# Kernel tuning notes

Hardware: AMD Instinct MI355X
Metric: run time of the kernel (lower is better)

## Reference

```python
import jax, jax.numpy as jnp
import numpy as np

N = 50000      # nodes
E = 400000     # edges (before self-loops)
G = 256        # graphs in batch
H = 2          # attention heads
C = 100        # out channels per head
F_IN = 336
SLOPE = 0.2    # PyG GATConv default negative_slope


def setup_inputs() -> dict:
    key = jax.random.key(0)
    ks = jax.random.split(key, 32)
    inp = {}
    inp['x'] = jax.random.normal(ks[0], (N, F_IN), dtype=jnp.float32)
    inp['edge_index'] = jax.random.randint(ks[1], (2, E), 0, N, dtype=jnp.int32)
    inp['batch'] = jnp.sort(jax.random.randint(ks[2], (N,), 0, G, dtype=jnp.int32))
    dims = [F_IN, 200, 200, 200, 200]
    k = 3
    for i in range(5):
        d = dims[i]
        inp[f'W{i+1}'] = jax.random.normal(ks[k], (d, H * C), dtype=jnp.float32) / float(np.sqrt(d)); k += 1
        inp[f'asrc{i+1}'] = jax.random.normal(ks[k], (H, C), dtype=jnp.float32) * 0.1; k += 1
        inp[f'adst{i+1}'] = jax.random.normal(ks[k], (H, C), dtype=jnp.float32) * 0.1; k += 1
        inp[f'bc{i+1}'] = jnp.zeros((H * C,), jnp.float32)
    for i, (a, b) in enumerate([(200, 100), (100, 100), (100, 29)]):
        inp[f'lw{i+1}'] = jax.random.normal(ks[k], (a, b), dtype=jnp.float32) / float(np.sqrt(a)); k += 1
        inp[f'lb{i+1}'] = jnp.zeros((b,), jnp.float32)
    return inp


def _gat(x, src, dst, W, a_s, a_d, b):
    # PyG GATConv (concat=True): per-head linear, additive attention,
    # softmax over incoming edges per destination node, weighted sum.
    h = (x @ W).reshape(-1, H, C)                      # [N,H,C]
    es = jnp.einsum('nhc,hc->nh', h, a_s)              # [N,H] src scores
    ed = jnp.einsum('nhc,hc->nh', h, a_d)              # [N,H] dst scores
    e = jax.nn.leaky_relu(es[src] + ed[dst], SLOPE)    # [E+N,H]
    m = jax.ops.segment_max(e, dst, num_segments=N)    # per-dest max (stable softmax)
    p = jnp.exp(e - m[dst])
    s = jax.ops.segment_sum(p, dst, num_segments=N)
    alpha = p / (s[dst] + 1e-16)                       # [E+N,H]
    msg = alpha[:, :, None] * h[src]                   # [E+N,H,C]
    out = jax.ops.segment_sum(msg, dst, num_segments=N)
    return out.reshape(-1, H * C) + b


def reference(x, edge_index, batch,
              W1, asrc1, adst1, bc1, W2, asrc2, adst2, bc2,
              W3, asrc3, adst3, bc3, W4, asrc4, adst4, bc4,
              W5, asrc5, adst5, bc5,
              lw1, lb1, lw2, lb2, lw3, lb3):
    loop = jnp.arange(N, dtype=edge_index.dtype)       # self-loops (PyG default)
    src = jnp.concatenate([edge_index[0], loop])
    dst = jnp.concatenate([edge_index[1], loop])
    for W, a_s, a_d, b in [(W1, asrc1, adst1, bc1), (W2, asrc2, adst2, bc2),
                           (W3, asrc3, adst3, bc3), (W4, asrc4, adst4, bc4),
                           (W5, asrc5, adst5, bc5)]:
        x = jax.nn.relu(_gat(x, src, dst, W, a_s, a_d, b))
    # global mean pool over nodes of each graph
    sums = jax.ops.segment_sum(x, batch, num_segments=G)
    cnt = jax.ops.segment_sum(jnp.ones((N, 1), x.dtype), batch, num_segments=G)
    x = sums / jnp.maximum(cnt, 1.0)
    x = jax.nn.relu(x @ lw1 + lb1)
    x = jax.nn.relu(x @ lw2 + lb2)
    return x @ lw3 + lb3
```

## Files before the change

### kernel.cpp

```cpp
#include <hip/hip_runtime.h>
#include <hip/hip_bf16.h>
#include <math.h>

#define F_IN   336
#define HC     200
#define Cch    100
#define SLOPE  0.2f
#define SCAN_BS 256

#define NPAD   224
#define KP0    352
#define KP1    224

using short8   = __attribute__((ext_vector_type(8))) short;
using float4v  = __attribute__((ext_vector_type(4))) float;
using ushort4v = __attribute__((ext_vector_type(4))) unsigned short;
using float2v  = __attribute__((ext_vector_type(2))) float;

__device__ inline unsigned short rne_bf16(float v) {
    unsigned int u = __float_as_uint(v);
    return (unsigned short)((u + 0x7fffu + ((u >> 16) & 1u)) >> 16);
}
__device__ inline void split_bf(float v, unsigned short& hi, unsigned short& lo) {
    hi = rne_bf16(v);
    float hv = __uint_as_float(((unsigned int)hi) << 16);
    lo = rne_bf16(v - hv);
}

__global__ void init_deg(int* deg, int n) {
    int i = blockIdx.x * 256 + threadIdx.x;
    if (i < n) deg[i] = 1;
}

__global__ void count_deg(const int* __restrict__ dst, int* deg, int e) {
    int i = blockIdx.x * 256 + threadIdx.x;
    if (i < e) atomicAdd(&deg[dst[i]], 1);
}

__global__ void scan_block(const int* __restrict__ deg, int* incl, int* bsums, int n) {
    __shared__ int sm[SCAN_BS];
    int i = blockIdx.x * SCAN_BS + threadIdx.x;
    int v = (i < n) ? deg[i] : 0;
    sm[threadIdx.x] = v;
    __syncthreads();
    for (int off = 1; off < SCAN_BS; off <<= 1) {
        int t = (threadIdx.x >= off) ? sm[threadIdx.x - off] : 0;
        __syncthreads();
        sm[threadIdx.x] += t;
        __syncthreads();
    }
    if (i < n) incl[i] = sm[threadIdx.x];
    if (threadIdx.x == SCAN_BS - 1) bsums[blockIdx.x] = sm[threadIdx.x];
}

__global__ void scan_sums(int* bsums, int nb) {
    __shared__ int sm[SCAN_BS];
    int v = (threadIdx.x < nb) ? bsums[threadIdx.x] : 0;
    sm[threadIdx.x] = v;
    __syncthreads();
    for (int off = 1; off < SCAN_BS; off <<= 1) {
        int t = (threadIdx.x >= off) ? sm[threadIdx.x - off] : 0;
        __syncthreads();
        sm[threadIdx.x] += t;
        __syncthreads();
    }
    if (threadIdx.x < nb) bsums[threadIdx.x] = sm[threadIdx.x] - v;
}

__global__ void scan_final(const int* __restrict__ incl, const int* __restrict__ deg,
                           const int* __restrict__ bsums, int* row_ptr, int* cursor, int n) {
    int i = blockIdx.x * SCAN_BS + threadIdx.x;
    if (i < n) {
        int inc = incl[i] + bsums[i / SCAN_BS];
        int ex  = inc - deg[i];
        row_ptr[i] = ex;
        cursor[i]  = ex;
        if (i == n - 1) row_ptr[n] = inc;
    }
}

__global__ void fill_csr(const int* __restrict__ src, const int* __restrict__ dst,
                         int* cursor, int* col_src, int e, int n) {
    int i = blockIdx.x * 256 + threadIdx.x;
    int te = e + n;
    if (i >= te) return;
    int s, d;
    if (i < e) { s = src[i]; d = dst[i]; }
    else       { s = i - e;  d = i - e; }
    int pos = atomicAdd(&cursor[d], 1);
    col_src[pos] = s;
}

__global__ void conv_x(const float* __restrict__ x, unsigned short* __restrict__ Ah,
                       unsigned short* __restrict__ Al, int n_nodes) {
    int i = blockIdx.x * 256 + threadIdx.x;
    int tot = n_nodes * KP0;
    if (i >= tot) return;
    int row = i / KP0, col = i - row * KP0;
    float v = (col < F_IN) ? x[(size_t)row * F_IN + col] : 0.f;
    unsigned short hi, lo;
    split_bf(v, hi, lo);
    Ah[i] = hi; Al[i] = lo;
}

__global__ void conv_w(const float* __restrict__ W, unsigned short* __restrict__ Bh,
                       unsigned short* __restrict__ Bl, int K, int Kp) {
    int i = blockIdx.x * 256 + threadIdx.x;
    int tot = NPAD * Kp;
    if (i >= tot) return;
    int n = i / Kp, k = i - n * Kp;
    float v = (n < HC && k < K) ? W[(size_t)k * HC + n] : 0.f;
    unsigned short hi, lo;
    split_bf(v, hi, lo);
    Bh[i] = hi; Bl[i] = lo;
}

#define LDK 40
__global__ __launch_bounds__(256, 2) void gemm_split(
    const unsigned short* __restrict__ Ah, const unsigned short* __restrict__ Al,
    const unsigned short* __restrict__ Bh, const unsigned short* __restrict__ Bl,
    float* __restrict__ h, int M, int Kp)
{
    __shared__ unsigned short As[2][64][LDK];
    __shared__ unsigned short Bs[2][NPAD][LDK];
    int tid  = threadIdx.x;
    int wave = tid >> 6, lane = tid & 63;
    int quad = lane >> 4, l16 = lane & 15;
    int wm = (wave >> 1) * 32;
    int wn = (wave & 1) * 112;
    int r0 = blockIdx.x * 64;

    float4v acc[2][7];
#pragma unroll
    for (int mt = 0; mt < 2; mt++)
#pragma unroll
        for (int nt = 0; nt < 7; nt++)
            acc[mt][nt] = (float4v){0.f, 0.f, 0.f, 0.f};

    for (int k0 = 0; k0 < Kp; k0 += 32) {
#pragma unroll
        for (int i = 0; i < 2; i++) {
            int c = tid + 256 * i;
            int s = c >> 8;
            int cc = c & 255;
            int row = cc >> 2, kc = (cc & 3) * 8;
            const unsigned short* g = s ? Al : Ah;
            uint4 v = make_uint4(0u, 0u, 0u, 0u);
            int gr = r0 + row;
            if (gr < M) v = *(const uint4*)(g + (size_t)gr * Kp + k0 + kc);
            *(uint4*)&As[s][row][kc] = v;
        }
#pragma unroll
        for (int i = 0; i < 7; i++) {
            int c = tid + 256 * i;
            int s = (c >= 896) ? 1 : 0;
            int cc = c - s * 896;
            int row = cc >> 2, kc = (cc & 3) * 8;
            const unsigned short* g = s ? Bl : Bh;
            *(uint4*)&Bs[s][row][kc] = *(const uint4*)(g + (size_t)row * Kp + k0 + kc);
        }
        __syncthreads();

        short8 a_h[2], a_l[2];
#pragma unroll
        for (int mt = 0; mt < 2; mt++) {
            a_h[mt] = *(const short8*)&As[0][wm + mt * 16 + l16][quad * 8];
            a_l[mt] = *(const short8*)&As[1][wm + mt * 16 + l16][quad * 8];
        }
#pragma unroll
        for (int nt = 0; nt < 7; nt++) {
            short8 b_h = *(const short8*)&Bs[0][wn + nt * 16 + l16][quad * 8];
            short8 b_l = *(const short8*)&Bs[1][wn + nt * 16 + l16][quad * 8];
#pragma unroll
            for (int mt = 0; mt < 2; mt++) {
                acc[mt][nt] = __builtin_amdgcn_mfma_f32_16x16x32_bf16(a_h[mt], b_h, acc[mt][nt], 0, 0, 0);
                acc[mt][nt] = __builtin_amdgcn_mfma_f32_16x16x32_bf16(a_h[mt], b_l, acc[mt][nt], 0, 0, 0);
                acc[mt][nt] = __builtin_amdgcn_mfma_f32_16x16x32_bf16(a_l[mt], b_h, acc[mt][nt], 0, 0, 0);
            }
        }
        __syncthreads();
    }

#pragma unroll
    for (int mt = 0; mt < 2; mt++) {
#pragma unroll
        for (int nt = 0; nt < 7; nt++) {
            int col = wn + nt * 16 + l16;
            if (col >= HC) continue;
#pragma unroll
            for (int r = 0; r < 4; r++) {
                int grow = r0 + wm + mt * 16 + quad * 4 + r;
                if (grow < M) h[(size_t)grow * HC + col] = acc[mt][nt][r];
            }
        }
    }
}

__global__ __launch_bounds__(256) void gat_scores(
    const float* __restrict__ h, const float* __restrict__ asrc, const float* __restrict__ adst,
    float* __restrict__ es, float* __restrict__ ed, int n_nodes)
{
    int wave = threadIdx.x >> 6, lane = threadIdx.x & 63;
    int n = blockIdx.x * 4 + wave;
    if (n >= n_nodes) return;
#pragma unroll
    for (int hd = 0; hd < 2; hd++) {
        const float* hr = h + (size_t)n * HC + hd * Cch;
        const float* as = asrc + hd * Cch;
        const float* ad = adst + hd * Cch;
        float v = hr[lane];
        float ps = v * as[lane];
        float pd = v * ad[lane];
        if (lane < Cch - 64) {
            float v2 = hr[lane + 64];
            ps += v2 * as[lane + 64];
            pd += v2 * ad[lane + 64];
        }
        for (int off = 32; off > 0; off >>= 1) {
            ps += __shfl_down(ps, off);
            pd += __shfl_down(pd, off);
        }
        if (lane == 0) { es[n * 2 + hd] = ps; ed[n * 2 + hd] = pd; }
    }
}

__global__ __launch_bounds__(256) void gat_alpha(
    const float* __restrict__ es, const float* __restrict__ ed,
    const int* __restrict__ row_ptr, const int* __restrict__ col_src,
    float* __restrict__ pbuf, float* __restrict__ linv, int n_nodes)
{
    int n = blockIdx.x * 256 + threadIdx.x;
    if (n >= n_nodes) return;
    int e0 = row_ptr[n], e1 = row_ptr[n + 1];
    float ed0 = ed[n * 2], ed1 = ed[n * 2 + 1];
    float m0 = -INFINITY, m1 = -INFINITY;
    for (int e = e0; e < e1; e++) {
        int s = col_src[e];
        float s0 = es[s * 2] + ed0, s1 = es[s * 2 + 1] + ed1;
        s0 = s0 > 0.f ? s0 : SLOPE * s0;
        s1 = s1 > 0.f ? s1 : SLOPE * s1;
        m0 = fmaxf(m0, s0); m1 = fmaxf(m1, s1);
    }
    float l0 = 0.f, l1 = 0.f;
    for (int e = e0; e < e1; e++) {
        int s = col_src[e];
        float s0 = es[s * 2] + ed0, s1 = es[s * 2 + 1] + ed1;
        s0 = s0 > 0.f ? s0 : SLOPE * s0;
        s1 = s1 > 0.f ? s1 : SLOPE * s1;
        float p0 = __expf(s0 - m0), p1 = __expf(s1 - m1);
        l0 += p0; l1 += p1;
        float2v pp = {p0, p1};
        *(float2v*)&pbuf[(size_t)e * 2] = pp;
    }
    linv[n * 2]     = 1.f / (l0 + 1e-16f);
    linv[n * 2 + 1] = 1.f / (l1 + 1e-16f);
}

template<bool WF, bool WB>
__global__ __launch_bounds__(256) void gat_gather(
    const float* __restrict__ h, const float* __restrict__ pbuf, const float* __restrict__ linv,
    const int* __restrict__ row_ptr, const int* __restrict__ col_src,
    const float* __restrict__ bias, float* __restrict__ outF,
    unsigned short* __restrict__ oh, unsigned short* __restrict__ ol, int n_nodes)
{
    int wave = threadIdx.x >> 6, lane = threadIdx.x & 63;
    int n = blockIdx.x * 4 + wave;
    if (n >= n_nodes) return;
    int e0 = row_ptr[n], e1 = row_ptr[n + 1];
    bool act  = lane < 50;
    int  hsel = (lane >= 25) ? 1 : 0;

    float4v a0 = {0.f, 0.f, 0.f, 0.f}, a1 = {0.f, 0.f, 0.f, 0.f};
    float4v a2 = {0.f, 0.f, 0.f, 0.f}, a3 = {0.f, 0.f, 0.f, 0.f};

    for (int cbase = e0; cbase < e1; cbase += 64) {
        int cnt = e1 - cbase; if (cnt > 64) cnt = 64;
        int   sidx = 0;
        float px = 0.f, py = 0.f;
        if (lane < cnt) {
            sidx = col_src[cbase + lane];
            float2v pp = *(const float2v*)&pbuf[(size_t)(cbase + lane) * 2];
            px = pp.x; py = pp.y;
        }
        int j = 0;
        for (; j + 4 <= cnt; j += 4) {
            int s0 = __shfl(sidx, j + 0), s1 = __shfl(sidx, j + 1);
            int s2 = __shfl(sidx, j + 2), s3 = __shfl(sidx, j + 3);
            float x0 = __shfl(px, j + 0), y0 = __shfl(py, j + 0);
            float x1 = __shfl(px, j + 1), y1 = __shfl(py, j + 1);
            float x2 = __shfl(px, j + 2), y2 = __shfl(py, j + 2);
            float x3 = __shfl(px, j + 3), y3 = __shfl(py, j + 3);
            float p0 = hsel ? y0 : x0;
            float p1 = hsel ? y1 : x1;
            float p2 = hsel ? y2 : x2;
            float p3 = hsel ? y3 : x3;
            if (act) {
                float4v v0 = *(const float4v*)(h + (size_t)s0 * HC + lane * 4);
                float4v v1 = *(const float4v*)(h + (size_t)s1 * HC + lane * 4);
                float4v v2 = *(const float4v*)(h + (size_t)s2 * HC + lane * 4);
                float4v v3 = *(const float4v*)(h + (size_t)s3 * HC + lane * 4);
                a0.x += p0 * v0.x; a0.y += p0 * v0.y; a0.z += p0 * v0.z; a0.w += p0 * v0.w;
                a1.x += p1 * v1.x; a1.y += p1 * v1.y; a1.z += p1 * v1.z; a1.w += p1 * v1.w;
                a2.x += p2 * v2.x; a2.y += p2 * v2.y; a2.z += p2 * v2.z; a2.w += p2 * v2.w;
                a3.x += p3 * v3.x; a3.y += p3 * v3.y; a3.z += p3 * v3.z; a3.w += p3 * v3.w;
            }
        }
        for (; j < cnt; j++) {
            int s0 = __shfl(sidx, j);
            float x0 = __shfl(px, j), y0 = __shfl(py, j);
            float p0 = hsel ? y0 : x0;
            if (act) {
                float4v v0 = *(const float4v*)(h + (size_t)s0 * HC + lane * 4);
                a0.x += p0 * v0.x; a0.y += p0 * v0.y; a0.z += p0 * v0.z; a0.w += p0 * v0.w;
            }
        }
    }
    float4v acc;
    acc.x = (a0.x + a1.x) + (a2.x + a3.x);
    acc.y = (a0.y + a1.y) + (a2.y + a3.y);
    acc.z = (a0.z + a1.z) + (a2.z + a3.z);
    acc.w = (a0.w + a1.w) + (a2.w + a3.w);

    float li = linv[n * 2 + hsel];
    if (act) {
        float4v bb = *(const float4v*)(bias + lane * 4);
        float4v r;
        r.x = fmaxf(acc.x * li + bb.x, 0.f);
        r.y = fmaxf(acc.y * li + bb.y, 0.f);
        r.z = fmaxf(acc.z * li + bb.z, 0.f);
        r.w = fmaxf(acc.w * li + bb.w, 0.f);
        if (WF) {
            __builtin_nontemporal_store(r, (float4v*)(outF + (size_t)n * HC + lane * 4));
        }
        if (WB) {
            ushort4v hv, lv;
            split_bf(r.x, ((unsigned short*)&hv)[0], ((unsigned short*)&lv)[0]);
            split_bf(r.y, ((unsigned short*)&hv)[1], ((unsigned short*)&lv)[1]);
            split_bf(r.z, ((unsigned short*)&hv)[2], ((unsigned short*)&lv)[2]);
            split_bf(r.w, ((unsigned short*)&hv)[3], ((unsigned short*)&lv)[3]);
            size_t b = (size_t)n * NPAD + lane * 4;
            __builtin_nontemporal_store(hv, (ushort4v*)(oh + b));
            __builtin_nontemporal_store(lv, (ushort4v*)(ol + b));
        }
    } else if (WB && lane < 56) {
        ushort4v z = {0, 0, 0, 0};
        size_t b = (size_t)n * NPAD + lane * 4;
        __builtin_nontemporal_store(z, (ushort4v*)(oh + b));
        __builtin_nontemporal_store(z, (ushort4v*)(ol + b));
    }
}

__global__ void pool_zero(float* pool, int tot) {
    int i = blockIdx.x * 256 + threadIdx.x;
    if (i < tot) pool[i] = 0.f;
}

__global__ __launch_bounds__(256) void pool_part(
    const float* __restrict__ x, const int* __restrict__ batch,
    float* __restrict__ pool, int n_nodes)
{
    int wave = threadIdx.x >> 6, lane = threadIdx.x & 63;
    int base = (blockIdx.x * 4 + wave) * 16;
    if (base >= n_nodes) return;
    bool act = lane < 50;
    int end = base + 16; if (end > n_nodes) end = n_nodes;
    float4v acc = {0.f, 0.f, 0.f, 0.f};
    int curg = batch[base];
    for (int n = base; n < end; n++) {
        int g = batch[n];
        if (g != curg) {
            if (act) {
                float* pp = pool + (size_t)curg * HC + lane * 4;
                atomicAdd(pp + 0, acc.x); atomicAdd(pp + 1, acc.y);
                atomicAdd(pp + 2, acc.z); atomicAdd(pp + 3, acc.w);
            }
            acc = (float4v){0.f, 0.f, 0.f, 0.f};
            curg = g;
        }
        if (act) {
            float4v v = *(const float4v*)(x + (size_t)n * HC + lane * 4);
            acc.x += v.x; acc.y += v.y; acc.z += v.z; acc.w += v.w;
        }
    }
    if (act) {
        float* pp = pool + (size_t)curg * HC + lane * 4;
        atomicAdd(pp + 0, acc.x); atomicAdd(pp + 1, acc.y);
        atomicAdd(pp + 2, acc.z); atomicAdd(pp + 3, acc.w);
    }
}

__global__ void pool_div(float* pool, const int* __restrict__ gstart, int g_count) {
    int i = blockIdx.x * 256 + threadIdx.x;
    if (i >= g_count * HC) return;
    int g = i / HC;
    float cnt = (float)(gstart[g + 1] - gstart[g]);
    pool[i] /= fmaxf(cnt, 1.f);
}

__global__ void graph_bounds(const int* __restrict__ batch, int* gstart, int n, int g) {
    int i = blockIdx.x * 256 + threadIdx.x;
    if (i >= n) return;
    int b = batch[i];
    int bp = (i == 0) ? -1 : batch[i - 1];
    for (int q = bp + 1; q <= b; q++) gstart[q] = i;
    if (i == n - 1) for (int q = b + 1; q <= g; q++) gstart[q] = n;
}

template<int KIN, int KOUT, bool RELU>
__global__ __launch_bounds__(128) void mlp(
    const float* __restrict__ in, const float* __restrict__ W, const float* __restrict__ b,
    float* __restrict__ out)
{
    __shared__ float xi[KIN];
    int g = blockIdx.x;
    for (int k = threadIdx.x; k < KIN; k += blockDim.x) xi[k] = in[g * KIN + k];
    __syncthreads();
    int j = threadIdx.x;
    if (j < KOUT) {
        float s = b[j];
        for (int k = 0; k < KIN; k++) s = fmaf(xi[k], W[k * KOUT + j], s);
        if (RELU) s = fmaxf(s, 0.f);
        out[g * KOUT + j] = s;
    }
}

extern "C" void kernel_launch(void* const* d_in, const int* in_sizes, int n_in,
                              void* d_out, int out_size, void* d_ws, size_t ws_size,
                              hipStream_t stream) {
    const float* x     = (const float*)d_in[0];
    const int*   ei    = (const int*)d_in[1];
    const int*   batch = (const int*)d_in[2];
    const float *W[5], *asrc[5], *adst[5], *bc[5];
    for (int i = 0; i < 5; i++) {
        W[i]    = (const float*)d_in[3 + i * 4];
        asrc[i] = (const float*)d_in[4 + i * 4];
        adst[i] = (const float*)d_in[5 + i * 4];
        bc[i]   = (const float*)d_in[6 + i * 4];
    }
    const float* lw1 = (const float*)d_in[23];
    const float* lb1 = (const float*)d_in[24];
    const float* lw2 = (const float*)d_in[25];
    const float* lb2 = (const float*)d_in[26];
    const float* lw3 = (const float*)d_in[27];
    const float* lb3 = (const float*)d_in[28];
    float* out = (float*)d_out;

    const int N  = in_sizes[0] / F_IN;
    const int E  = in_sizes[1] / 2;
    const int G  = out_size / 29;
    const int TE = E + N;
    const int* esrc = ei;
    const int* edst = ei + E;

    char* p = (char*)d_ws;
    auto carve = [&](size_t bytes) { void* r = (void*)p; p += ((bytes + 255) / 256) * 256; return r; };
    float*          hbuf = (float*)carve((size_t)N * HC * 4);
    unsigned short* Ah   = (unsigned short*)carve((size_t)N * KP0 * 2);
    unsigned short* Al   = (unsigned short*)carve((size_t)N * KP0 * 2);
    float*          outF = (float*)Ah;
    unsigned short* Wth  = (unsigned short*)carve((size_t)NPAD * KP0 * 2);
    unsigned short* Wtl  = (unsigned short*)carve((size_t)NPAD * KP0 * 2);
    float* es_     = (float*)carve((size_t)N * 2 * 4);
    float* ed_     = (float*)carve((size_t)N * 2 * 4);
    float* pbuf    = (float*)carve((size_t)TE * 2 * 4);
    float* linv    = (float*)carve((size_t)N * 2 * 4);
    int*   deg     = (int*)carve((size_t)N * 4);
    int*   incl    = (int*)carve((size_t)N * 4);
    int*   bsums   = (int*)carve(SCAN_BS * 4);
    int*   row_ptr = (int*)carve((size_t)(N + 1) * 4);
    int*   cursor  = (int*)carve((size_t)N * 4);
    int*   col_src = (int*)carve((size_t)TE * 4);
    int*   gstart  = (int*)carve((size_t)(G + 1) * 4);
    float* pool    = (float*)carve((size_t)G * HC * 4);
    float* t1      = (float*)carve((size_t)G * 100 * 4);
    float* t2      = (float*)carve((size_t)G * 100 * 4);

    const int nBlkN   = (N + 255) / 256;
    const int nBlkE   = (E + 255) / 256;
    const int nBlkTE  = (TE + 255) / 256;
    const int nScanB  = (N + SCAN_BS - 1) / SCAN_BS;
    const int nWaveB  = (N + 3) / 4;
    const int nGemmB  = (N + 63) / 64;
    const int nPoolB  = (N + 63) / 64;

    init_deg<<<nBlkN, 256, 0, stream>>>(deg, N);
    count_deg<<<nBlkE, 256, 0, stream>>>(edst, deg, E);
    scan_block<<<nScanB, SCAN_BS, 0, stream>>>(deg, incl, bsums, N);
    scan_sums<<<1, SCAN_BS, 0, stream>>>(bsums, nScanB);
    scan_final<<<nScanB, SCAN_BS, 0, stream>>>(incl, deg, bsums, row_ptr, cursor, N);
    fill_csr<<<nBlkTE, 256, 0, stream>>>(esrc, edst, cursor, col_src, E, N);

    conv_x<<<(N * KP0 + 255) / 256, 256, 0, stream>>>(x, Ah, Al, N);

    for (int L = 0; L < 5; L++) {
        int K  = (L == 0) ? F_IN : HC;
        int Kp = (L == 0) ? KP0 : KP1;
        conv_w<<<(NPAD * Kp + 255) / 256, 256, 0, stream>>>(W[L], Wth, Wtl, K, Kp);
        gemm_split<<<nGemmB, 256, 0, stream>>>(Ah, Al, Wth, Wtl, hbuf, N, Kp);
        gat_scores<<<nWaveB, 256, 0, stream>>>(hbuf, asrc[L], adst[L], es_, ed_, N);
        gat_alpha<<<nBlkN, 256, 0, stream>>>(es_, ed_, row_ptr, col_src, pbuf, linv, N);
        if (L < 4)
            gat_gather<false, true><<<nWaveB, 256, 0, stream>>>(hbuf, pbuf, linv, row_ptr, col_src,
                                                                bc[L], nullptr, Ah, Al, N);
        else
            gat_gather<true, false><<<nWaveB, 256, 0, stream>>>(hbuf, pbuf, linv, row_ptr, col_src,
                                                                bc[L], outF, nullptr, nullptr, N);
    }

    graph_bounds<<<nBlkN, 256, 0, stream>>>(batch, gstart, N, G);
    pool_zero<<<(G * HC + 255) / 256, 256, 0, stream>>>(pool, G * HC);
    pool_part<<<nPoolB, 256, 0, stream>>>(outF, batch, pool, N);
    pool_div<<<(G * HC + 255) / 256, 256, 0, stream>>>(pool, gstart, G);

    mlp<200, 100, true ><<<G, 128, 0, stream>>>(pool, lw1, lb1, t1);
    mlp<100, 100, true ><<<G, 128, 0, stream>>>(t1, lw2, lb2, t2);
    mlp<100, 29,  false><<<G, 128, 0, stream>>>(t2, lw3, lb3, out);
}
```

Before: 951.7 us.

## Fuse attention score dot products into GEMM epilogue and parallelize softmax per node

The GEMM epilogue now computes the per-node source and destination attention scores, reducing across lanes with shuffles and across waves with LDS atomics, which removes the separate gat_scores kernel and its re-read of h. The per-node softmax kernel now assigns 16 lanes per node instead of one thread, stores the leaky-relu scores in the first pass and reads them back to avoid gathering es twice. conv_x is vectorized to float4 loads and ushort4 stores. The changes add epilogue register pressure and atomic traffic in the GEMM, and the float4 load relies on the 336-column rows being 16-byte aligned.

```diff
diff --git a/kernel.cpp b/kernel.cpp
--- a/kernel.cpp
+++ b/kernel.cpp
@@ -93,14 +93,22 @@
 
 __global__ void conv_x(const float* __restrict__ x, unsigned short* __restrict__ Ah,
                        unsigned short* __restrict__ Al, int n_nodes) {
-    int i = blockIdx.x * 256 + threadIdx.x;
-    int tot = n_nodes * KP0;
+    const int GPR = KP0 / 4;
+    int i = blockIdx.x * 256 + threadIdx.x;
+    int tot = n_nodes * GPR;
     if (i >= tot) return;
-    int row = i / KP0, col = i - row * KP0;
-    float v = (col < F_IN) ? x[(size_t)row * F_IN + col] : 0.f;
-    unsigned short hi, lo;
-    split_bf(v, hi, lo);
-    Ah[i] = hi; Al[i] = lo;
+    int row = i / GPR, g4 = i - row * GPR;
+    int col = g4 * 4;
+    float4v v = {0.f, 0.f, 0.f, 0.f};
+    if (col < F_IN) v = *(const float4v*)(x + (size_t)row * F_IN + col);
+    ushort4v hv, lv;
+    split_bf(v.x, ((unsigned short*)&hv)[0], ((unsigned short*)&lv)[0]);
+    split_bf(v.y, ((unsigned short*)&hv)[1], ((unsigned short*)&lv)[1]);
+    split_bf(v.z, ((unsigned short*)&hv)[2], ((unsigned short*)&lv)[2]);
+    split_bf(v.w, ((unsigned short*)&hv)[3], ((unsigned short*)&lv)[3]);
+    size_t b = (size_t)row * KP0 + col;
+    *(ushort4v*)(Ah + b) = hv;
+    *(ushort4v*)(Al + b) = lv;
 }
 
 __global__ void conv_w(const float* __restrict__ W, unsigned short* __restrict__ Bh,
@@ -119,16 +127,21 @@
 __global__ __launch_bounds__(256, 2) void gemm_split(
     const unsigned short* __restrict__ Ah, const unsigned short* __restrict__ Al,
     const unsigned short* __restrict__ Bh, const unsigned short* __restrict__ Bl,
-    float* __restrict__ h, int M, int Kp)
+    const float* __restrict__ asrc, const float* __restrict__ adst,
+    float* __restrict__ h, float* __restrict__ es, float* __restrict__ ed,
+    int M, int Kp)
 {
     __shared__ unsigned short As[2][64][LDK];
     __shared__ unsigned short Bs[2][NPAD][LDK];
+    __shared__ float sc[64][4];
     int tid  = threadIdx.x;
     int wave = tid >> 6, lane = tid & 63;
     int quad = lane >> 4, l16 = lane & 15;
     int wm = (wave >> 1) * 32;
     int wn = (wave & 1) * 112;
     int r0 = blockIdx.x * 64;
+
+    ((float*)sc)[tid] = 0.f;
 
     float4v acc[2][7];
 #pragma unroll
@@ -181,79 +194,113 @@
         __syncthreads();
     }
 
+    float asc[7], adc[7];
+    bool  vld[7];
+    bool  hd1[7];
+#pragma unroll
+    for (int nt = 0; nt < 7; nt++) {
+        int col = wn + nt * 16 + l16;
+        vld[nt] = col < HC;
+        hd1[nt] = col >= Cch;
+        asc[nt] = vld[nt] ? asrc[col] : 0.f;
+        adc[nt] = vld[nt] ? adst[col] : 0.f;
+    }
+
 #pragma unroll
     for (int mt = 0; mt < 2; mt++) {
+        float p[4][4];
+#pragma unroll
+        for (int r = 0; r < 4; r++)
+#pragma unroll
+            for (int t = 0; t < 4; t++) p[r][t] = 0.f;
 #pragma unroll
         for (int nt = 0; nt < 7; nt++) {
             int col = wn + nt * 16 + l16;
-            if (col >= HC) continue;
 #pragma unroll
             for (int r = 0; r < 4; r++) {
+                float v = acc[mt][nt][r];
                 int grow = r0 + wm + mt * 16 + quad * 4 + r;
-                if (grow < M) h[(size_t)grow * HC + col] = acc[mt][nt][r];
+                if (vld[nt] && grow < M) h[(size_t)grow * HC + col] = v;
+                float va = v * asc[nt], vd = v * adc[nt];
+                p[r][0] += hd1[nt] ? 0.f : va;
+                p[r][1] += hd1[nt] ? va  : 0.f;
+                p[r][2] += hd1[nt] ? 0.f : vd;
+                p[r][3] += hd1[nt] ? vd  : 0.f;
             }
         }
-    }
-}
-
-__global__ __launch_bounds__(256) void gat_scores(
-    const float* __restrict__ h, const float* __restrict__ asrc, const float* __restrict__ adst,
-    float* __restrict__ es, float* __restrict__ ed, int n_nodes)
-{
-    int wave = threadIdx.x >> 6, lane = threadIdx.x & 63;
-    int n = blockIdx.x * 4 + wave;
-    if (n >= n_nodes) return;
-#pragma unroll
-    for (int hd = 0; hd < 2; hd++) {
-        const float* hr = h + (size_t)n * HC + hd * Cch;
-        const float* as = asrc + hd * Cch;
-        const float* ad = adst + hd * Cch;
-        float v = hr[lane];
-        float ps = v * as[lane];
-        float pd = v * ad[lane];
-        if (lane < Cch - 64) {
-            float v2 = hr[lane + 64];
-            ps += v2 * as[lane + 64];
-            pd += v2 * ad[lane + 64];
-        }
-        for (int off = 32; off > 0; off >>= 1) {
-            ps += __shfl_down(ps, off);
-            pd += __shfl_down(pd, off);
-        }
-        if (lane == 0) { es[n * 2 + hd] = ps; ed[n * 2 + hd] = pd; }
-    }
-}
-
-__global__ __launch_bounds__(256) void gat_alpha(
+#pragma unroll
+        for (int off = 1; off < 16; off <<= 1)
+#pragma unroll
+            for (int r = 0; r < 4; r++)
+#pragma unroll
+                for (int t = 0; t < 4; t++)
+                    p[r][t] += __shfl_xor(p[r][t], off);
+        if (l16 == 0) {
+            int lrow = wm + mt * 16 + quad * 4;
+#pragma unroll
+            for (int r = 0; r < 4; r++)
+#pragma unroll
+                for (int t = 0; t < 4; t++)
+                    atomicAdd(&sc[lrow + r][t], p[r][t]);
+        }
+    }
+    __syncthreads();
+    if (tid < 64) {
+        int grow = r0 + tid;
+        if (grow < M) {
+            es[grow * 2 + 0] = sc[tid][0];
+            es[grow * 2 + 1] = sc[tid][1];
+            ed[grow * 2 + 0] = sc[tid][2];
+            ed[grow * 2 + 1] = sc[tid][3];
+        }
+    }
+}
+
+__global__ __launch_bounds__(256) void gat_alpha_par(
     const float* __restrict__ es, const float* __restrict__ ed,
     const int* __restrict__ row_ptr, const int* __restrict__ col_src,
     float* __restrict__ pbuf, float* __restrict__ linv, int n_nodes)
 {
-    int n = blockIdx.x * 256 + threadIdx.x;
+    int tid = threadIdx.x;
+    int sub = tid >> 4;
+    int l   = tid & 15;
+    int n = blockIdx.x * 16 + sub;
     if (n >= n_nodes) return;
     int e0 = row_ptr[n], e1 = row_ptr[n + 1];
     float ed0 = ed[n * 2], ed1 = ed[n * 2 + 1];
     float m0 = -INFINITY, m1 = -INFINITY;
-    for (int e = e0; e < e1; e++) {
+    for (int e = e0 + l; e < e1; e += 16) {
         int s = col_src[e];
-        float s0 = es[s * 2] + ed0, s1 = es[s * 2 + 1] + ed1;
+        float2v q = *(const float2v*)&es[s * 2];
+        float s0 = q.x + ed0, s1 = q.y + ed1;
         s0 = s0 > 0.f ? s0 : SLOPE * s0;
         s1 = s1 > 0.f ? s1 : SLOPE * s1;
         m0 = fmaxf(m0, s0); m1 = fmaxf(m1, s1);
+        float2v w = {s0, s1};
+        *(float2v*)&pbuf[(size_t)e * 2] = w;
+    }
+#pragma unroll
+    for (int off = 1; off < 16; off <<= 1) {
+        m0 = fmaxf(m0, __shfl_xor(m0, off));
+        m1 = fmaxf(m1, __shfl_xor(m1, off));
     }
     float l0 = 0.f, l1 = 0.f;
-    for (int e = e0; e < e1; e++) {
-        int s = col_src[e];
-        float s0 = es[s * 2] + ed0, s1 = es[s * 2 + 1] + ed1;
-        s0 = s0 > 0.f ? s0 : SLOPE * s0;
-        s1 = s1 > 0.f ? s1 : SLOPE * s1;
-        float p0 = __expf(s0 - m0), p1 = __expf(s1 - m1);
+    for (int e = e0 + l; e < e1; e += 16) {
+        float2v w = *(const float2v*)&pbuf[(size_t)e * 2];
+        float p0 = __expf(w.x - m0), p1 = __expf(w.y - m1);
         l0 += p0; l1 += p1;
         float2v pp = {p0, p1};
         *(float2v*)&pbuf[(size_t)e * 2] = pp;
     }
-    linv[n * 2]     = 1.f / (l0 + 1e-16f);
-    linv[n * 2 + 1] = 1.f / (l1 + 1e-16f);
+#pragma unroll
+    for (int off = 1; off < 16; off <<= 1) {
+        l0 += __shfl_xor(l0, off);
+        l1 += __shfl_xor(l1, off);
+    }
+    if (l == 0) {
+        linv[n * 2]     = 1.f / (l0 + 1e-16f);
+        linv[n * 2 + 1] = 1.f / (l1 + 1e-16f);
+    }
 }
 
 template<bool WF, bool WB>
@@ -482,6 +529,7 @@
     const int nWaveB  = (N + 3) / 4;
     const int nGemmB  = (N + 63) / 64;
     const int nPoolB  = (N + 63) / 64;
+    const int nAlphaB = (N + 15) / 16;
 
     init_deg<<<nBlkN, 256, 0, stream>>>(deg, N);
     count_deg<<<nBlkE, 256, 0, stream>>>(edst, deg, E);
@@ -490,15 +538,15 @@
     scan_final<<<nScanB, SCAN_BS, 0, stream>>>(incl, deg, bsums, row_ptr, cursor, N);
     fill_csr<<<nBlkTE, 256, 0, stream>>>(esrc, edst, cursor, col_src, E, N);
 
-    conv_x<<<(N * KP0 + 255) / 256, 256, 0, stream>>>(x, Ah, Al, N);
+    conv_x<<<(N * (KP0 / 4) + 255) / 256, 256, 0, stream>>>(x, Ah, Al, N);
 
     for (int L = 0; L < 5; L++) {
         int K  = (L == 0) ? F_IN : HC;
         int Kp = (L == 0) ? KP0 : KP1;
         conv_w<<<(NPAD * Kp + 255) / 256, 256, 0, stream>>>(W[L], Wth, Wtl, K, Kp);
-        gemm_split<<<nGemmB, 256, 0, stream>>>(Ah, Al, Wth, Wtl, hbuf, N, Kp);
-        gat_scores<<<nWaveB, 256, 0, stream>>>(hbuf, asrc[L], adst[L], es_, ed_, N);
-        gat_alpha<<<nBlkN, 256, 0, stream>>>(es_, ed_, row_ptr, col_src, pbuf, linv, N);
+        gemm_split<<<nGemmB, 256, 0, stream>>>(Ah, Al, Wth, Wtl, asrc[L], adst[L],
+                                               hbuf, es_, ed_, N, Kp);
+        gat_alpha_par<<<nAlphaB, 256, 0, stream>>>(es_, ed_, row_ptr, col_src, pbuf, linv, N);
         if (L < 4)
             gat_gather<false, true><<<nWaveB, 256, 0, stream>>>(hbuf, pbuf, linv, row_ptr, col_src,
                                                                 bc[L], nullptr, Ah, Al, N);
```

New measurement: 834.8 us. 12.3% less time.
